# Kernel optimization log

Measured on AMD Instinct MI355X. Metric: run time of the kernel, lower is better.

The kernel has to match this reference:

```python
import jax, jax.numpy as jnp
import numpy as np

H1 = 36
H2 = 1


def _lstm(x, W_ih, W_hh, b_ih, b_hh, H):
    # x: [B, T, D]; W_ih: [4H, D]; W_hh: [4H, H]; biases: [4H]
    # PyTorch gate order: i, f, g, o
    B, T, _ = x.shape
    xg = jnp.einsum('btd,gd->btg', x, W_ih) + (b_ih + b_hh)  # [B, T, 4H]

    def step(carry, xg_t):
        h, c = carry
        g = xg_t + h @ W_hh.T  # [B, 4H]
        i, f, gc, o = jnp.split(g, 4, axis=-1)
        c = jax.nn.sigmoid(f) * c + jax.nn.sigmoid(i) * jnp.tanh(gc)
        h = jax.nn.sigmoid(o) * jnp.tanh(c)
        return (h, c), h

    h0 = jnp.zeros((B, H), x.dtype)
    (_, _), hs = jax.lax.scan(step, (h0, h0), jnp.swapaxes(xg, 0, 1))
    return jnp.swapaxes(hs, 0, 1)  # [B, T, H]


def setup_inputs() -> dict:
    key = jax.random.key(0)
    ks = jax.random.split(key, 9)
    B, T = 2048, 2048
    s1 = 1.0 / np.sqrt(H1)
    s2 = 1.0  # 1/sqrt(hidden_size=1)
    return {
        'x': jax.random.normal(ks[0], (B, T, 1), dtype=jnp.float32),
        'W_ih1': jax.random.uniform(ks[1], (4 * H1, 1), jnp.float32, -s1, s1),
        'W_hh1': jax.random.uniform(ks[2], (4 * H1, H1), jnp.float32, -s1, s1),
        'b_ih1': jax.random.uniform(ks[3], (4 * H1,), jnp.float32, -s1, s1),
        'b_hh1': jax.random.uniform(ks[4], (4 * H1,), jnp.float32, -s1, s1),
        'W_ih2': jax.random.uniform(ks[5], (4 * H2, H1), jnp.float32, -s2, s2),
        'W_hh2': jax.random.uniform(ks[6], (4 * H2, H2), jnp.float32, -s2, s2),
        'b_ih2': jax.random.uniform(ks[7], (4 * H2,), jnp.float32, -s2, s2),
        'b_hh2': jax.random.uniform(ks[8], (4 * H2,), jnp.float32, -s2, s2),
    }


def reference(x, W_ih1, W_hh1, b_ih1, b_hh1, W_ih2, W_hh2, b_ih2, b_hh2):
    h1 = _lstm(x, W_ih1, W_hh1, b_ih1, b_hh1, H1)   # [B, T, 36]
    h1 = jax.nn.relu(h1)
    out = _lstm(h1, W_ih2, W_hh2, b_ih2, b_hh2, H2)  # [B, T, 1]
    return out
```

## Files before the change

kernel.cpp:

```cpp
#include <hip/hip_runtime.h>

namespace {

constexpr int T_LEN = 2048;
constexpr int B_TOT = 2048;
constexpr int H1 = 36;
constexpr int NB = 16;
constexpr int BLOCK = 640;
constexpr int RS = 72;

typedef _Float16 f16x8 __attribute__((ext_vector_type(8)));
typedef _Float16 h16x2 __attribute__((ext_vector_type(2)));
typedef float f32x4 __attribute__((ext_vector_type(4)));

__device__ __forceinline__ float fdot2(float wb, float hb, float acc) {
#if __has_builtin(__builtin_amdgcn_fdot2)
  return __builtin_amdgcn_fdot2(__builtin_bit_cast(h16x2, wb),
                                __builtin_bit_cast(h16x2, hb), acc, false);
#else
  float d;
  asm("v_dot2_f32_f16 %0, %1, %2, %3" : "=v"(d) : "v"(wb), "v"(hb), "0"(acc));
  return d;
#endif
}
__device__ __forceinline__ float pack2h(float a, float b) {
  h16x2 t = {(_Float16)a, (_Float16)b};
  return __builtin_bit_cast(float, t);
}
template <int CTRL>
__device__ __forceinline__ float qb(float v) {
  return __builtin_bit_cast(
      float, __builtin_amdgcn_update_dpp(0, __builtin_bit_cast(int, v), CTRL,
                                         0xf, 0xf, true));
}
__device__ __forceinline__ float fexp2(float x) { return __builtin_amdgcn_exp2f(x); }
__device__ __forceinline__ float frcp(float x) { return __builtin_amdgcn_rcpf(x); }

__device__ __forceinline__ float lstm_unit(float pi, float pf, float pg, float po,
                                           float& cS) {
  const float Ei = fexp2(pi);
  const float Ef = fexp2(pf);
  const float Eg = fexp2(pg);
  const float Eo = fexp2(po);
  const float F = frcp(1.f + Ef);
  const float Rig = frcp((1.f + Ei) * (1.f + Eg));
  const float numg = fmaf(Eg, 2.88539008f, -2.88539008f);
  cS = fmaf(F, cS, numg * Rig);
  const float Ec = fexp2(cS);
  const float Roc = frcp((1.f + Eo) * (1.f + Ec));
  return (1.f - Ec) * Roc;
}

__device__ __forceinline__ void step_sync() {
  asm volatile("s_waitcnt lgkmcnt(0)" ::: "memory");
  __builtin_amdgcn_s_barrier();
  __builtin_amdgcn_sched_barrier(0);
  asm volatile("" ::: "memory");
}

__global__ __launch_bounds__(BLOCK) void lstm2_kernel(
    const float* __restrict__ x, const float* __restrict__ Wih1,
    const float* __restrict__ Whh1, const float* __restrict__ bih1,
    const float* __restrict__ bhh1, const float* __restrict__ Wih2,
    const float* __restrict__ Whh2, const float* __restrict__ bih2,
    const float* __restrict__ bhh2, float* __restrict__ out)
{
  __shared__ __align__(16) _Float16 lds[2][2][NB][RS];

  const int tid = threadIdx.x;
  const int wid = tid >> 6;
  const int lane = tid & 63;
  const int m = lane & 15;
  const int q = lane >> 4;
  const int g0 = blockIdx.x * NB;
  const bool isA = wid < 9;

  for (int i = tid; i < 2 * 2 * NB * RS; i += BLOCK)
    ((_Float16*)lds)[i] = (_Float16)0.f;
  __syncthreads();
  if (tid < NB) {
    lds[0][0][tid][38] = (_Float16)1.f;
    lds[0][0][tid][39] = (_Float16)1.f;
    lds[1][0][tid][38] = (_Float16)1.f;
    lds[1][0][tid][39] = (_Float16)1.f;
    const float x0 = x[(size_t)(g0 + tid) * T_LEN];
    const _Float16 xh0 = (_Float16)x0;
    lds[1][0][tid][36] = xh0;
    lds[1][0][tid][37] = (_Float16)(x0 - (float)xh0);
  }
  __syncthreads();

  f16x8 A0 = {}, A1 = {};
  float c1 = 0.f;
  int ku = 0;
  if (isA) {
    const int u0 = wid * 4;
    ku = u0 + q;
    const float sga = ((m & 3) == 2) ? -2.88539008f : -1.44269504f;
    const int ra = (m & 3) * H1 + (u0 + (m >> 2));
#pragma unroll
    for (int j = 0; j < 8; ++j)
      A0[j] = (_Float16)(sga * Whh1[ra * H1 + q * 8 + j]);
#pragma unroll
    for (int j = 0; j < 8; ++j) A1[j] = (_Float16)0.f;
    if (q == 0) {
#pragma unroll
      for (int j = 0; j < 4; ++j)
        A1[j] = (_Float16)(sga * Whh1[ra * H1 + 32 + j]);
      const _Float16 wih = (_Float16)(sga * Wih1[ra]);
      A1[4] = wih;
      A1[5] = wih;
      const float bb = sga * (bih1[ra] + bhh1[ra]);
      const _Float16 bh = (_Float16)bb;
      A1[6] = bh;
      A1[7] = (_Float16)(bb - (float)bh);
    }
  }

  const float* xc = nullptr;
  float4 qx = make_float4(0.f, 0.f, 0.f, 0.f);
  if (wid == 8) {
    xc = x + (size_t)(g0 + m) * T_LEN;
    qx = *(const float4*)xc;
  }

  const int lb = lane >> 2, lg = lane & 3;
  float w2[18];
  float whg = 0.f, b2 = 0.f, c2S = 0.f, h2 = 0.f;
  float* outp = nullptr;
#pragma unroll
  for (int k = 0; k < 18; ++k) w2[k] = 0.f;
  if (wid == 9) {
    const float s2 = (lg == 2) ? -2.88539008f : -1.44269504f;
    const float* wr = Wih2 + lg * H1;
#pragma unroll
    for (int k = 0; k < 18; ++k)
      w2[k] = pack2h(s2 * wr[2 * k], s2 * wr[2 * k + 1]);
    whg = s2 * Whh2[lg];
    b2 = s2 * (bih2[lg] + bhh2[lg]);
    outp = out + (size_t)(g0 + lb) * T_LEN;
  }

  float4 ov = make_float4(0.f, 0.f, 0.f, 0.f);
  const f32x4 z4 = {0.f, 0.f, 0.f, 0.f};

  auto step = [&](int i, int s, float xw) {
    const int ib = (s + 1) & 1;
    const int wb = s & 1;
    if (isA) {
      const f16x8 B0 = *(const f16x8*)&lds[ib][0][m][q * 8];
      const f16x8 B1 = *(const f16x8*)&lds[ib][0][m][32 + q * 8];
      const f32x4 cc1 = __builtin_amdgcn_mfma_f32_16x16x32_f16(A0, B0, z4, 0, 0, 0);
      const f32x4 cc2 = __builtin_amdgcn_mfma_f32_16x16x32_f16(A1, B1, z4, 0, 0, 0);
      const float h = lstm_unit(cc1[0] + cc2[0], cc1[1] + cc2[1],
                                cc1[2] + cc2[2], cc1[3] + cc2[3], c1);
      const _Float16 hh = (_Float16)h;
      lds[wb][0][m][ku] = hh;
      lds[wb][1][m][ku] = (hh > (_Float16)0.f) ? hh : (_Float16)0.f;
      if (wid == 8 && q == 0) {
        const _Float16 xh = (_Float16)xw;
        h16x2 xp = {xh, (_Float16)(xw - (float)xh)};
        *(h16x2*)&lds[wb][0][m][36] = xp;
      }
    } else if (i > 0) {
      const char* rp = (const char*)&lds[ib][1][lb][0];
      const float4 r0 = *(const float4*)rp;
      const float4 r1 = *(const float4*)(rp + 16);
      const float4 r2 = *(const float4*)(rp + 32);
      const float4 r3 = *(const float4*)(rp + 48);
      const float2 r4 = *(const float2*)(rp + 64);
      const float f[18] = {r0.x, r0.y, r0.z, r0.w, r1.x, r1.y, r1.z, r1.w,
                           r2.x, r2.y, r2.z, r2.w, r3.x, r3.y, r3.z, r3.w,
                           r4.x, r4.y};
      float a0 = fdot2(w2[0], f[0], fmaf(h2, whg, b2));
      float a1 = fdot2(w2[1], f[1], 0.f);
      float a2 = fdot2(w2[2], f[2], 0.f);
      float a3 = fdot2(w2[3], f[3], 0.f);
#pragma unroll
      for (int k = 4; k < 16; k += 4) {
        a0 = fdot2(w2[k], f[k], a0);
        a1 = fdot2(w2[k + 1], f[k + 1], a1);
        a2 = fdot2(w2[k + 2], f[k + 2], a2);
        a3 = fdot2(w2[k + 3], f[k + 3], a3);
      }
      a0 = fdot2(w2[16], f[16], a0);
      a1 = fdot2(w2[17], f[17], a1);
      const float pre = (a0 + a2) + (a1 + a3);
      const float pI = qb<0x00>(pre);
      const float pF = qb<0x55>(pre);
      const float pG = qb<0xAA>(pre);
      const float pO = qb<0xFF>(pre);
      h2 = lstm_unit(pI, pF, pG, pO, c2S);
      if (s == 1) ov.x = h2;
      else if (s == 2) ov.y = h2;
      else if (s == 3) ov.z = h2;
      else {
        ov.w = h2;
        if (lg == 0) *(float4*)(outp + (i - 4)) = ov;
      }
    }
    step_sync();
  };

  for (int i0 = 0; i0 < T_LEN; i0 += 4) {
    float4 qn = qx;
    if (wid == 8) {
      const int tn = (i0 + 4 < T_LEN) ? (i0 + 4) : (T_LEN - 4);
      qn = *(const float4*)(xc + tn);
    }
    step(i0 + 0, 0, qx.y);
    step(i0 + 1, 1, qx.z);
    step(i0 + 2, 2, qx.w);
    step(i0 + 3, 3, qn.x);
    qx = qn;
  }
  step(T_LEN, 0, qx.y);
}

}

extern "C" void kernel_launch(void* const* d_in, const int* in_sizes, int n_in,
                              void* d_out, int out_size, void* d_ws, size_t ws_size,
                              hipStream_t stream) {
  const float* x    = (const float*)d_in[0];
  const float* Wih1 = (const float*)d_in[1];
  const float* Whh1 = (const float*)d_in[2];
  const float* bih1 = (const float*)d_in[3];
  const float* bhh1 = (const float*)d_in[4];
  const float* Wih2 = (const float*)d_in[5];
  const float* Whh2 = (const float*)d_in[6];
  const float* bih2 = (const float*)d_in[7];
  const float* bhh2 = (const float*)d_in[8];
  float* out = (float*)d_out;

  dim3 grid(B_TOT / NB);
  dim3 block(BLOCK);
  hipLaunchKernelGGL(lstm2_kernel, grid, block, 0, stream,
                     x, Wih1, Whh1, bih1, bhh1, Wih2, Whh2, bih2, bhh2, out);
}
```

Baseline: 788.9 us.

## Drop separate ReLU LDS copy, apply packed ReLU in layer-2 wave, move x feed

```diff
diff --git a/kernel.cpp b/kernel.cpp
--- a/kernel.cpp
+++ b/kernel.cpp
@@ -32,6 +32,11 @@
   return __builtin_bit_cast(
       float, __builtin_amdgcn_update_dpp(0, __builtin_bit_cast(int, v), CTRL,
                                          0xf, 0xf, true));
+}
+__device__ __forceinline__ float pkrelu(float v) {
+  float r;
+  asm("v_pk_max_f16 %0, %1, %2" : "=v"(r) : "v"(v), "v"(0.f));
+  return r;
 }
 __device__ __forceinline__ float fexp2(float x) { return __builtin_amdgcn_exp2f(x); }
 __device__ __forceinline__ float frcp(float x) { return __builtin_amdgcn_rcpf(x); }
@@ -65,7 +70,7 @@
     const float* __restrict__ Whh2, const float* __restrict__ bih2,
     const float* __restrict__ bhh2, float* __restrict__ out)
 {
-  __shared__ __align__(16) _Float16 lds[2][2][NB][RS];
+  __shared__ __align__(16) _Float16 lds[2][NB][RS];
 
   const int tid = threadIdx.x;
   const int wid = tid >> 6;
@@ -75,18 +80,18 @@
   const int g0 = blockIdx.x * NB;
   const bool isA = wid < 9;
 
-  for (int i = tid; i < 2 * 2 * NB * RS; i += BLOCK)
+  for (int i = tid; i < 2 * NB * RS; i += BLOCK)
     ((_Float16*)lds)[i] = (_Float16)0.f;
   __syncthreads();
   if (tid < NB) {
-    lds[0][0][tid][38] = (_Float16)1.f;
-    lds[0][0][tid][39] = (_Float16)1.f;
-    lds[1][0][tid][38] = (_Float16)1.f;
-    lds[1][0][tid][39] = (_Float16)1.f;
+    lds[0][tid][38] = (_Float16)1.f;
+    lds[0][tid][39] = (_Float16)1.f;
+    lds[1][tid][38] = (_Float16)1.f;
+    lds[1][tid][39] = (_Float16)1.f;
     const float x0 = x[(size_t)(g0 + tid) * T_LEN];
     const _Float16 xh0 = (_Float16)x0;
-    lds[1][0][tid][36] = xh0;
-    lds[1][0][tid][37] = (_Float16)(x0 - (float)xh0);
+    lds[1][tid][36] = xh0;
+    lds[1][tid][37] = (_Float16)(x0 - (float)xh0);
   }
   __syncthreads();
 
@@ -117,17 +122,12 @@
     }
   }
 
-  const float* xc = nullptr;
-  float4 qx = make_float4(0.f, 0.f, 0.f, 0.f);
-  if (wid == 8) {
-    xc = x + (size_t)(g0 + m) * T_LEN;
-    qx = *(const float4*)xc;
-  }
-
   const int lb = lane >> 2, lg = lane & 3;
   float w2[18];
   float whg = 0.f, b2 = 0.f, c2S = 0.f, h2 = 0.f;
   float* outp = nullptr;
+  const float* xc = nullptr;
+  float4 qx = make_float4(0.f, 0.f, 0.f, 0.f);
 #pragma unroll
   for (int k = 0; k < 18; ++k) w2[k] = 0.f;
   if (wid == 9) {
@@ -139,6 +139,8 @@
     whg = s2 * Whh2[lg];
     b2 = s2 * (bih2[lg] + bhh2[lg]);
     outp = out + (size_t)(g0 + lb) * T_LEN;
+    xc = x + (size_t)(g0 + lb) * T_LEN;
+    qx = *(const float4*)xc;
   }
 
   float4 ov = make_float4(0.f, 0.f, 0.f, 0.f);
@@ -148,55 +150,62 @@
     const int ib = (s + 1) & 1;
     const int wb = s & 1;
     if (isA) {
-      const f16x8 B0 = *(const f16x8*)&lds[ib][0][m][q * 8];
-      const f16x8 B1 = *(const f16x8*)&lds[ib][0][m][32 + q * 8];
+      const f16x8 B0 = *(const f16x8*)&lds[ib][m][q * 8];
+      f16x8 B1;
+#pragma unroll
+      for (int j = 0; j < 8; ++j) B1[j] = (_Float16)0.f;
+      if (q == 0)
+        B1 = *(const f16x8*)&lds[ib][m][32];
       const f32x4 cc1 = __builtin_amdgcn_mfma_f32_16x16x32_f16(A0, B0, z4, 0, 0, 0);
       const f32x4 cc2 = __builtin_amdgcn_mfma_f32_16x16x32_f16(A1, B1, z4, 0, 0, 0);
       const float h = lstm_unit(cc1[0] + cc2[0], cc1[1] + cc2[1],
                                 cc1[2] + cc2[2], cc1[3] + cc2[3], c1);
-      const _Float16 hh = (_Float16)h;
-      lds[wb][0][m][ku] = hh;
-      lds[wb][1][m][ku] = (hh > (_Float16)0.f) ? hh : (_Float16)0.f;
-      if (wid == 8 && q == 0) {
+      lds[wb][m][ku] = (_Float16)h;
+    } else {
+      if (lg == 0) {
         const _Float16 xh = (_Float16)xw;
         h16x2 xp = {xh, (_Float16)(xw - (float)xh)};
-        *(h16x2*)&lds[wb][0][m][36] = xp;
+        *(h16x2*)&lds[wb][lb][36] = xp;
       }
-    } else if (i > 0) {
-      const char* rp = (const char*)&lds[ib][1][lb][0];
-      const float4 r0 = *(const float4*)rp;
-      const float4 r1 = *(const float4*)(rp + 16);
-      const float4 r2 = *(const float4*)(rp + 32);
-      const float4 r3 = *(const float4*)(rp + 48);
-      const float2 r4 = *(const float2*)(rp + 64);
-      const float f[18] = {r0.x, r0.y, r0.z, r0.w, r1.x, r1.y, r1.z, r1.w,
-                           r2.x, r2.y, r2.z, r2.w, r3.x, r3.y, r3.z, r3.w,
-                           r4.x, r4.y};
-      float a0 = fdot2(w2[0], f[0], fmaf(h2, whg, b2));
-      float a1 = fdot2(w2[1], f[1], 0.f);
-      float a2 = fdot2(w2[2], f[2], 0.f);
-      float a3 = fdot2(w2[3], f[3], 0.f);
-#pragma unroll
-      for (int k = 4; k < 16; k += 4) {
-        a0 = fdot2(w2[k], f[k], a0);
-        a1 = fdot2(w2[k + 1], f[k + 1], a1);
-        a2 = fdot2(w2[k + 2], f[k + 2], a2);
-        a3 = fdot2(w2[k + 3], f[k + 3], a3);
-      }
-      a0 = fdot2(w2[16], f[16], a0);
-      a1 = fdot2(w2[17], f[17], a1);
-      const float pre = (a0 + a2) + (a1 + a3);
-      const float pI = qb<0x00>(pre);
-      const float pF = qb<0x55>(pre);
-      const float pG = qb<0xAA>(pre);
-      const float pO = qb<0xFF>(pre);
-      h2 = lstm_unit(pI, pF, pG, pO, c2S);
-      if (s == 1) ov.x = h2;
-      else if (s == 2) ov.y = h2;
-      else if (s == 3) ov.z = h2;
-      else {
-        ov.w = h2;
-        if (lg == 0) *(float4*)(outp + (i - 4)) = ov;
+      if (i > 0) {
+        const char* rp = (const char*)&lds[ib][lb][0];
+        const float4 r0 = *(const float4*)rp;
+        const float4 r1 = *(const float4*)(rp + 16);
+        const float4 r2 = *(const float4*)(rp + 32);
+        const float4 r3 = *(const float4*)(rp + 48);
+        const float2 r4 = *(const float2*)(rp + 64);
+        const float f[18] = {
+            pkrelu(r0.x), pkrelu(r0.y), pkrelu(r0.z), pkrelu(r0.w),
+            pkrelu(r1.x), pkrelu(r1.y), pkrelu(r1.z), pkrelu(r1.w),
+            pkrelu(r2.x), pkrelu(r2.y), pkrelu(r2.z), pkrelu(r2.w),
+            pkrelu(r3.x), pkrelu(r3.y), pkrelu(r3.z), pkrelu(r3.w),
+            pkrelu(r4.x), pkrelu(r4.y)};
+        float a0 = fdot2(w2[0], f[0], fmaf(h2, whg, b2));
+        float a1 = fdot2(w2[1], f[1], 0.f);
+        float a2 = fdot2(w2[2], f[2], 0.f);
+        float a3 = fdot2(w2[3], f[3], 0.f);
+#pragma unroll
+        for (int k = 4; k < 16; k += 4) {
+          a0 = fdot2(w2[k], f[k], a0);
+          a1 = fdot2(w2[k + 1], f[k + 1], a1);
+          a2 = fdot2(w2[k + 2], f[k + 2], a2);
+          a3 = fdot2(w2[k + 3], f[k + 3], a3);
+        }
+        a0 = fdot2(w2[16], f[16], a0);
+        a1 = fdot2(w2[17], f[17], a1);
+        const float pre = (a0 + a2) + (a1 + a3);
+        const float pI = qb<0x00>(pre);
+        const float pF = qb<0x55>(pre);
+        const float pG = qb<0xAA>(pre);
+        const float pO = qb<0xFF>(pre);
+        h2 = lstm_unit(pI, pF, pG, pO, c2S);
+        if (s == 1) ov.x = h2;
+        else if (s == 2) ov.y = h2;
+        else if (s == 3) ov.z = h2;
+        else {
+          ov.w = h2;
+          if (lg == 0) *(float4*)(outp + (i - 4)) = ov;
+        }
       }
     }
     step_sync();
@@ -204,7 +213,7 @@
 
   for (int i0 = 0; i0 < T_LEN; i0 += 4) {
     float4 qn = qx;
-    if (wid == 8) {
+    if (wid == 9) {
       const int tn = (i0 + 4 < T_LEN) ? (i0 + 4) : (T_LEN - 4);
       qn = *(const float4*)(xc + tn);
     }
```

After: 885.1 us. 1.12x slower.
